# Kernel tuning notes

Hardware: AMD Instinct MI355X
Metric: run time of the kernel (lower is better)

The kernel has to match this reference:

```python
import jax, jax.numpy as jnp
import numpy as np

N_EMBED = 384
T_MAX = 256
EPS = 1e-5


def layer_norm(x, gamma, beta):
    mu = jnp.mean(x, axis=-1, keepdims=True)
    var = jnp.mean(jnp.square(x - mu), axis=-1, keepdims=True)
    return (x - mu) * jax.lax.rsqrt(var + EPS) * gamma + beta


def setup_inputs() -> dict:
    key = jax.random.key(0)
    ks = jax.random.split(key, 12)
    B, T, C = 128, 256, N_EMBED
    s = lambda fan_in: 1.0 / np.sqrt(fan_in)
    return {
        "x": jax.random.normal(ks[0], (B, T, C), dtype=jnp.float32),
        "W_attn": jax.random.uniform(ks[1], (C, 3 * C), minval=-s(C), maxval=s(C), dtype=jnp.float32),
        "b_attn": jax.random.uniform(ks[2], (3 * C,), minval=-s(C), maxval=s(C), dtype=jnp.float32),
        "W_proj": jax.random.uniform(ks[3], (C, C), minval=-s(C), maxval=s(C), dtype=jnp.float32),
        "b_proj": jax.random.uniform(ks[4], (C,), minval=-s(C), maxval=s(C), dtype=jnp.float32),
        "ln1_g": jnp.ones((C,), jnp.float32),
        "ln1_b": jnp.zeros((C,), jnp.float32),
        "ln2_g": jnp.ones((C,), jnp.float32),
        "ln2_b": jnp.zeros((C,), jnp.float32),
        "W1": jax.random.uniform(ks[5], (C, 4 * C), minval=-s(C), maxval=s(C), dtype=jnp.float32),
        "b1": jax.random.uniform(ks[6], (4 * C,), minval=-s(C), maxval=s(C), dtype=jnp.float32),
        "W2": jax.random.uniform(ks[7], (4 * C, C), minval=-s(4 * C), maxval=s(4 * C), dtype=jnp.float32),
        "b2": jax.random.uniform(ks[8], (4 * C,)[:1] and (C,), minval=-s(4 * C), maxval=s(4 * C), dtype=jnp.float32),
    }


def reference(x, W_attn, b_attn, W_proj, b_proj, ln1_g, ln1_b, ln2_g, ln2_b, W1, b1, W2, b2):
    B, T, C = x.shape
    # --- pre-LN single-head causal self-attention ---
    h = layer_norm(x, ln1_g, ln1_b)
    qkv = h @ W_attn + b_attn                      # [B,T,3C]
    q, k, v = jnp.split(qkv, 3, axis=-1)           # each [B,T,C]
    att = jnp.einsum('btc,bsc->bts', q, k) * (1.0 / jnp.sqrt(jnp.float32(C)))
    causal = jnp.tril(jnp.ones((T, T), bool))
    att = jnp.where(causal, att, -jnp.inf)
    att = jax.nn.softmax(att, axis=-1)             # dropout is identity (eval)
    y = jnp.einsum('bts,bsc->btc', att, v)
    x = x + (y @ W_proj + b_proj)
    # --- pre-LN MLP ---
    h2 = layer_norm(x, ln2_g, ln2_b)
    x = x + (jax.nn.relu(h2 @ W1 + b1) @ W2 + b2)
    return x
```

## Files before the change

### kernel.cpp

```cpp
#include <hip/hip_runtime.h>
#include <hip/hip_bf16.h>

#define C_EMB 384
#define T_SEQ 256
#define B_BATCH 128
#define M_ROWS (B_BATCH * T_SEQ)
#define QKV_LD 1152
#define BK 64

typedef __bf16 bf16_8 __attribute__((ext_vector_type(8)));
typedef float f32x4 __attribute__((ext_vector_type(4)));

__device__ __forceinline__ void load16_lds(const __bf16* g, __bf16* l) {
    __builtin_amdgcn_global_load_lds(
        (const __attribute__((address_space(1))) unsigned int*)g,
        (__attribute__((address_space(3))) unsigned int*)l, 16, 0, 0);
}

__global__ __launch_bounds__(256) void cast_all_kernel(const float* __restrict__ Wa,
                                                       const float* __restrict__ Wp,
                                                       const float* __restrict__ W1,
                                                       const float* __restrict__ W2,
                                                       __bf16* __restrict__ Wa_t,
                                                       __bf16* __restrict__ Wp_t,
                                                       __bf16* __restrict__ W1_t,
                                                       __bf16* __restrict__ W2_t) {
    int bid = blockIdx.x;
    const float* W; __bf16* Wt; int K, N, tx_n;
    if (bid < 432)      { W = Wa; Wt = Wa_t; K = 384;  N = 1152; tx_n = 36; }
    else if (bid < 576) { bid -= 432; W = Wp; Wt = Wp_t; K = 384;  N = 384;  tx_n = 12; }
    else if (bid < 1152){ bid -= 576; W = W1; Wt = W1_t; K = 384;  N = 1536; tx_n = 48; }
    else                { bid -= 1152; W = W2; Wt = W2_t; K = 1536; N = 384;  tx_n = 12; }
    int n0 = (bid % tx_n) * 32, k0 = (bid / tx_n) * 32;

    __shared__ float t[32][33];
    int tx = threadIdx.x & 31, ty = threadIdx.x >> 5;
#pragma unroll
    for (int i = 0; i < 4; ++i)
        t[ty + i * 8][tx] = W[(size_t)(k0 + ty + i * 8) * N + n0 + tx];
    __syncthreads();
#pragma unroll
    for (int i = 0; i < 4; ++i) {
        int n = ty + i * 8;
        Wt[(size_t)(n0 + n) * K + k0 + tx] = (__bf16)t[tx][n];
    }
}

__global__ __launch_bounds__(384) void ln_kernel(const float* __restrict__ x,
                                                 const float* __restrict__ g,
                                                 const float* __restrict__ bta,
                                                 __bf16* __restrict__ out) {
    int row = blockIdx.x;
    int c = threadIdx.x;
    float v = x[(size_t)row * C_EMB + c];

    __shared__ float red[6];
    float s = v;
#pragma unroll
    for (int o = 32; o; o >>= 1) s += __shfl_down(s, o);
    if ((c & 63) == 0) red[c >> 6] = s;
    __syncthreads();
    float mu = (red[0] + red[1] + red[2] + red[3] + red[4] + red[5]) * (1.0f / C_EMB);

    float d = v - mu;
    float s2 = d * d;
#pragma unroll
    for (int o = 32; o; o >>= 1) s2 += __shfl_down(s2, o);
    __syncthreads();
    if ((c & 63) == 0) red[c >> 6] = s2;
    __syncthreads();
    float var = (red[0] + red[1] + red[2] + red[3] + red[4] + red[5]) * (1.0f / C_EMB);

    out[(size_t)row * C_EMB + c] = (__bf16)(d * rsqrtf(var + 1e-5f) * g[c] + bta[c]);
}

template <int TM, bool RELU, bool RESID, bool OUT_BF16>
__global__ __launch_bounds__(256) void mfma_gemm(const __bf16* __restrict__ A, int lda,
                                                 const __bf16* __restrict__ Bt, int ldb,
                                                 const float* __restrict__ bias,
                                                 const float* __restrict__ resid,
                                                 void* __restrict__ out_,
                                                 int N, int K) {
    constexpr int MI = TM / 32;
    constexpr int WROWS = TM / 2;
    __shared__ __align__(16) __bf16 As[2 * TM * 32];
    __shared__ __align__(16) __bf16 Bs[2 * 128 * 32];

    int tid = threadIdx.x;
    int wave = tid >> 6, lane = tid & 63;
    int wr = wave >> 1, wc = wave & 1;
    int quad = lane >> 4, l16 = lane & 15;
    int bm = blockIdx.y * TM, bn = blockIdx.x * 128;
    int lrow = lane >> 2, lcol = (lane & 3) * 8;

    f32x4 acc[MI][4] = {};

    for (int k0 = 0; k0 < K; k0 += BK) {
        const __bf16* Ab = A + (size_t)bm * lda + k0;
        const __bf16* Bb = Bt + (size_t)bn * ldb + k0;
#pragma unroll
        for (int p = 0; p < 2; ++p) {
#pragma unroll
            for (int i = 0; i < TM / 64; ++i) {
                int r0 = (i * 4 + wave) * 16;
                load16_lds(Ab + (size_t)(r0 + lrow) * lda + p * 32 + lcol,
                           &As[p * TM * 32 + r0 * 32]);
            }
#pragma unroll
            for (int i = 0; i < 2; ++i) {
                int r0 = (i * 4 + wave) * 16;
                load16_lds(Bb + (size_t)(r0 + lrow) * ldb + p * 32 + lcol,
                           &Bs[p * 128 * 32 + r0 * 32]);
            }
        }
        __syncthreads();

        bf16_8 af[MI][2], bf[4][2];
#pragma unroll
        for (int p = 0; p < 2; ++p) {
#pragma unroll
            for (int i = 0; i < MI; ++i)
                af[i][p] = *reinterpret_cast<const bf16_8*>(
                    &As[p * TM * 32 + (wr * WROWS + i * 16 + l16) * 32 + quad * 8]);
#pragma unroll
            for (int j = 0; j < 4; ++j)
                bf[j][p] = *reinterpret_cast<const bf16_8*>(
                    &Bs[p * 128 * 32 + (wc * 64 + j * 16 + l16) * 32 + quad * 8]);
        }
#pragma unroll
        for (int i = 0; i < MI; ++i)
#pragma unroll
            for (int j = 0; j < 4; ++j) {
                acc[i][j] = __builtin_amdgcn_mfma_f32_16x16x32_bf16(af[i][0], bf[j][0], acc[i][j], 0, 0, 0);
                acc[i][j] = __builtin_amdgcn_mfma_f32_16x16x32_bf16(af[i][1], bf[j][1], acc[i][j], 0, 0, 0);
            }
        __syncthreads();
    }

#pragma unroll
    for (int i = 0; i < MI; ++i) {
#pragma unroll
        for (int r = 0; r < 4; ++r) {
            int m = bm + wr * WROWS + i * 16 + quad * 4 + r;
#pragma unroll
            for (int j = 0; j < 4; ++j) {
                int n = bn + wc * 64 + j * 16 + l16;
                float v = acc[i][j][r] + bias[n];
                if (RELU) v = fmaxf(v, 0.0f);
                if (RESID) v += resid[(size_t)m * N + n];
                if (OUT_BF16)
                    ((__bf16*)out_)[(size_t)m * N + n] = (__bf16)v;
                else
                    ((float*)out_)[(size_t)m * N + n] = v;
            }
        }
    }
}

__global__ __launch_bounds__(256) void vt_kernel(const __bf16* __restrict__ qkv,
                                                 __bf16* __restrict__ Vt) {
    __shared__ __align__(16) __bf16 t[32][72];
    int b = blockIdx.z, c0 = blockIdx.x * 64, s0 = blockIdx.y * 32;
    int tid = threadIdx.x;

    int tx = tid & 7, ty = tid >> 3;
    const __bf16* src = qkv + ((size_t)b * T_SEQ + s0 + ty) * QKV_LD + 768 + c0 + tx * 8;
    *reinterpret_cast<float4*>(&t[ty][tx * 8]) = *reinterpret_cast<const float4*>(src);
    __syncthreads();

    int sx = tid & 3, cy = tid >> 2;
    __align__(16) __bf16 tmp[8];
#pragma unroll
    for (int j = 0; j < 8; ++j) tmp[j] = t[sx * 8 + j][cy];
    *reinterpret_cast<float4*>(&Vt[((size_t)b * C_EMB + c0 + cy) * T_SEQ + s0 + sx * 8]) =
        *reinterpret_cast<float4*>(tmp);
}

__global__ __launch_bounds__(256) void qk_mfma(const __bf16* __restrict__ qkv,
                                               float* __restrict__ S) {
    static const int TMt[3] = {0, 1, 1};
    static const int TNt[3] = {0, 0, 1};
    int b = blockIdx.y;
    int bm = TMt[blockIdx.x] * 128, bn = TNt[blockIdx.x] * 128;
    const __bf16* Ab0 = qkv + (size_t)b * T_SEQ * QKV_LD;
    const __bf16* Bb0 = Ab0 + 384;

    __shared__ __align__(16) __bf16 As[2 * 128 * 32];
    __shared__ __align__(16) __bf16 Bs[2 * 128 * 32];

    int tid = threadIdx.x;
    int wave = tid >> 6, lane = tid & 63;
    int wr = wave >> 1, wc = wave & 1;
    int quad = lane >> 4, l16 = lane & 15;
    int lrow = lane >> 2, lcol = (lane & 3) * 8;

    f32x4 acc[4][4] = {};

    for (int k0 = 0; k0 < C_EMB; k0 += BK) {
        const __bf16* Ab = Ab0 + (size_t)bm * QKV_LD + k0;
        const __bf16* Bb = Bb0 + (size_t)bn * QKV_LD + k0;
#pragma unroll
        for (int p = 0; p < 2; ++p)
#pragma unroll
            for (int i = 0; i < 2; ++i) {
                int r0 = (i * 4 + wave) * 16;
                load16_lds(Ab + (size_t)(r0 + lrow) * QKV_LD + p * 32 + lcol,
                           &As[p * 128 * 32 + r0 * 32]);
                load16_lds(Bb + (size_t)(r0 + lrow) * QKV_LD + p * 32 + lcol,
                           &Bs[p * 128 * 32 + r0 * 32]);
            }
        __syncthreads();

        bf16_8 af[4][2], bf[4][2];
#pragma unroll
        for (int p = 0; p < 2; ++p)
#pragma unroll
            for (int i = 0; i < 4; ++i) {
                af[i][p] = *reinterpret_cast<const bf16_8*>(
                    &As[p * 128 * 32 + (wr * 64 + i * 16 + l16) * 32 + quad * 8]);
                bf[i][p] = *reinterpret_cast<const bf16_8*>(
                    &Bs[p * 128 * 32 + (wc * 64 + i * 16 + l16) * 32 + quad * 8]);
            }
#pragma unroll
        for (int i = 0; i < 4; ++i)
#pragma unroll
            for (int j = 0; j < 4; ++j) {
                acc[i][j] = __builtin_amdgcn_mfma_f32_16x16x32_bf16(af[i][0], bf[j][0], acc[i][j], 0, 0, 0);
                acc[i][j] = __builtin_amdgcn_mfma_f32_16x16x32_bf16(af[i][1], bf[j][1], acc[i][j], 0, 0, 0);
            }
        __syncthreads();
    }

    float* Sb = S + (size_t)b * T_SEQ * T_SEQ;
#pragma unroll
    for (int i = 0; i < 4; ++i) {
#pragma unroll
        for (int r = 0; r < 4; ++r) {
            int m = bm + wr * 64 + i * 16 + quad * 4 + r;
#pragma unroll
            for (int j = 0; j < 4; ++j) {
                int n = bn + wc * 64 + j * 16 + l16;
                Sb[(size_t)m * T_SEQ + n] = acc[i][j][r] * 0.05103103630798288f;
            }
        }
    }
}

__global__ __launch_bounds__(256) void softmax_kernel(const float* __restrict__ S,
                                                      __bf16* __restrict__ P) {
    int row = blockIdx.x;
    int t = row & (T_SEQ - 1);
    int tid = threadIdx.x;
    const float* Sr = S + (size_t)row * T_SEQ;

    __shared__ float red[4];
    float sc = (tid <= t) ? Sr[tid] : -INFINITY;

    float mx = sc;
#pragma unroll
    for (int o = 32; o; o >>= 1) mx = fmaxf(mx, __shfl_down(mx, o));
    if ((tid & 63) == 0) red[tid >> 6] = mx;
    __syncthreads();
    mx = fmaxf(fmaxf(red[0], red[1]), fmaxf(red[2], red[3]));

    float p = (tid <= t) ? __expf(sc - mx) : 0.0f;
    float sm = p;
#pragma unroll
    for (int o = 32; o; o >>= 1) sm += __shfl_down(sm, o);
    __syncthreads();
    if ((tid & 63) == 0) red[tid >> 6] = sm;
    __syncthreads();
    sm = red[0] + red[1] + red[2] + red[3];

    P[(size_t)row * T_SEQ + tid] = (__bf16)(p / sm);
}

__global__ __launch_bounds__(256) void pv_mfma(const __bf16* __restrict__ P,
                                               const __bf16* __restrict__ Vt,
                                               __bf16* __restrict__ y) {
    int b = blockIdx.z;
    int bm = blockIdx.y * 128, bn = blockIdx.x * 128;
    const __bf16* Ab0 = P + (size_t)b * T_SEQ * T_SEQ;
    const __bf16* Bb0 = Vt + (size_t)b * C_EMB * T_SEQ;

    __shared__ __align__(16) __bf16 As[2 * 128 * 32];
    __shared__ __align__(16) __bf16 Bs[2 * 128 * 32];

    int tid = threadIdx.x;
    int wave = tid >> 6, lane = tid & 63;
    int wr = wave >> 1, wc = wave & 1;
    int quad = lane >> 4, l16 = lane & 15;
    int lrow = lane >> 2, lcol = (lane & 3) * 8;

    f32x4 acc[4][4] = {};

    int kmax = bm + 128;
    for (int k0 = 0; k0 < kmax; k0 += BK) {
        const __bf16* Ab = Ab0 + (size_t)bm * T_SEQ + k0;
        const __bf16* Bb = Bb0 + (size_t)bn * T_SEQ + k0;
#pragma unroll
        for (int p = 0; p < 2; ++p)
#pragma unroll
            for (int i = 0; i < 2; ++i) {
                int r0 = (i * 4 + wave) * 16;
                load16_lds(Ab + (size_t)(r0 + lrow) * T_SEQ + p * 32 + lcol,
                           &As[p * 128 * 32 + r0 * 32]);
                load16_lds(Bb + (size_t)(r0 + lrow) * T_SEQ + p * 32 + lcol,
                           &Bs[p * 128 * 32 + r0 * 32]);
            }
        __syncthreads();

        bf16_8 af[4][2], bf[4][2];
#pragma unroll
        for (int p = 0; p < 2; ++p)
#pragma unroll
            for (int i = 0; i < 4; ++i) {
                af[i][p] = *reinterpret_cast<const bf16_8*>(
                    &As[p * 128 * 32 + (wr * 64 + i * 16 + l16) * 32 + quad * 8]);
                bf[i][p] = *reinterpret_cast<const bf16_8*>(
                    &Bs[p * 128 * 32 + (wc * 64 + i * 16 + l16) * 32 + quad * 8]);
            }
#pragma unroll
        for (int i = 0; i < 4; ++i)
#pragma unroll
            for (int j = 0; j < 4; ++j) {
                acc[i][j] = __builtin_amdgcn_mfma_f32_16x16x32_bf16(af[i][0], bf[j][0], acc[i][j], 0, 0, 0);
                acc[i][j] = __builtin_amdgcn_mfma_f32_16x16x32_bf16(af[i][1], bf[j][1], acc[i][j], 0, 0, 0);
            }
        __syncthreads();
    }

#pragma unroll
    for (int i = 0; i < 4; ++i) {
#pragma unroll
        for (int r = 0; r < 4; ++r) {
            int m = bm + wr * 64 + i * 16 + quad * 4 + r;
#pragma unroll
            for (int j = 0; j < 4; ++j) {
                int n = bn + wc * 64 + j * 16 + l16;
                y[((size_t)b * T_SEQ + m) * C_EMB + n] = (__bf16)acc[i][j][r];
            }
        }
    }
}

extern "C" void kernel_launch(void* const* d_in, const int* in_sizes, int n_in,
                              void* d_out, int out_size, void* d_ws, size_t ws_size,
                              hipStream_t stream) {
    const float* x      = (const float*)d_in[0];
    const float* W_attn = (const float*)d_in[1];
    const float* b_attn = (const float*)d_in[2];
    const float* W_proj = (const float*)d_in[3];
    const float* b_proj = (const float*)d_in[4];
    const float* ln1_g  = (const float*)d_in[5];
    const float* ln1_b  = (const float*)d_in[6];
    const float* ln2_g  = (const float*)d_in[7];
    const float* ln2_b  = (const float*)d_in[8];
    const float* W1     = (const float*)d_in[9];
    const float* b1     = (const float*)d_in[10];
    const float* W2     = (const float*)d_in[11];
    const float* b2     = (const float*)d_in[12];
    float* out = (float*)d_out;

    __bf16* Wattn_t = (__bf16*)d_ws;
    __bf16* Wproj_t = Wattn_t + (size_t)1152 * 384;
    __bf16* W1_t    = Wproj_t + (size_t)384 * 384;
    __bf16* W2_t    = W1_t + (size_t)1536 * 384;
    __bf16* h       = W2_t + (size_t)384 * 1536;
    __bf16* yb      = h + (size_t)M_ROWS * 384;
    __bf16* qkv     = yb + (size_t)M_ROWS * 384;
    float*  S       = (float*)(qkv + (size_t)M_ROWS * QKV_LD);
    __bf16* Pb      = (__bf16*)(S + (size_t)B_BATCH * T_SEQ * T_SEQ);
    __bf16* Vt      = Pb + (size_t)B_BATCH * T_SEQ * T_SEQ;
    __bf16* ff      = qkv;

    cast_all_kernel<<<1728, 256, 0, stream>>>(W_attn, W_proj, W1, W2,
                                              Wattn_t, Wproj_t, W1_t, W2_t);

    ln_kernel<<<M_ROWS, 384, 0, stream>>>(x, ln1_g, ln1_b, h);
    mfma_gemm<128, false, false, true><<<dim3(1152 / 128, M_ROWS / 128), 256, 0, stream>>>(
        h, 384, Wattn_t, 384, b_attn, nullptr, qkv, 1152, 384);
    vt_kernel<<<dim3(C_EMB / 64, T_SEQ / 32, B_BATCH), 256, 0, stream>>>(qkv, Vt);
    qk_mfma<<<dim3(3, B_BATCH), 256, 0, stream>>>(qkv, S);
    softmax_kernel<<<M_ROWS, 256, 0, stream>>>(S, Pb);
    pv_mfma<<<dim3(C_EMB / 128, T_SEQ / 128, B_BATCH), 256, 0, stream>>>(Pb, Vt, yb);
    mfma_gemm<64, false, true, false><<<dim3(384 / 128, M_ROWS / 64), 256, 0, stream>>>(
        yb, 384, Wproj_t, 384, b_proj, x, out, 384, 384);
    ln_kernel<<<M_ROWS, 384, 0, stream>>>(out, ln2_g, ln2_b, h);
    mfma_gemm<128, true, false, true><<<dim3(1536 / 128, M_ROWS / 128), 256, 0, stream>>>(
        h, 384, W1_t, 384, b1, nullptr, ff, 1536, 384);
    mfma_gemm<64, false, true, false><<<dim3(384 / 128, M_ROWS / 64), 256, 0, stream>>>(
        ff, 1536, W2_t, 1536, b2, out, out, 384, 1536);
}
```

Baseline: 494.7 us.

## Fuse MLP up-projection, ReLU and down-projection into one kernel

Replaces the two MLP GEMM launches with a single kernel that computes a 64-row tile of h2@W1 in 64-column chunks. Each chunk gets bias and ReLU, is staged in LDS as bf16, and is immediately multiplied by the matching W2 slice, accumulating into registers. This removes writing and re-reading the 32768x1536 bf16 intermediate in global memory and one launch. In exchange, the W1/W2 tiles are re-streamed per row block with no double buffering, only 512 blocks run with many sync points, and register pressure is high (24 A fragments plus 24 accumulators per thread).

```diff
diff --git a/kernel.cpp b/kernel.cpp
--- a/kernel.cpp
+++ b/kernel.cpp
@@ -155,6 +155,128 @@
             }
         }
     }
+}
+
+__global__ __launch_bounds__(256, 2) void mlp_fused(const __bf16* __restrict__ h2,
+                                                    const __bf16* __restrict__ W1t,
+                                                    const __bf16* __restrict__ W2t,
+                                                    const float* __restrict__ b1,
+                                                    const float* __restrict__ b2,
+                                                    float* __restrict__ out) {
+    __shared__ __align__(16) __bf16 Bs[24576];
+    __shared__ __align__(16) __bf16 Ps[4096];
+
+    int tid = threadIdx.x;
+    int wave = tid >> 6, lane = tid & 63;
+    int wr = wave >> 1, wc = wave & 1;
+    int quad = lane >> 4, l16 = lane & 15;
+    int bm = blockIdx.x * 64;
+
+    int srow = lane >> 3;
+    int sunit = (lane & 7) ^ srow;
+
+    bf16_8 af1[2][12];
+    {
+        const __bf16* h0 = h2 + (size_t)(bm + wr * 32 + l16) * C_EMB + quad * 8;
+#pragma unroll
+        for (int i = 0; i < 2; ++i)
+#pragma unroll
+            for (int p = 0; p < 12; ++p)
+                af1[i][p] = *reinterpret_cast<const bf16_8*>(h0 + i * 16 * C_EMB + p * 32);
+    }
+
+    f32x4 acc2[2][12] = {};
+
+    for (int c = 0; c < 24; ++c) {
+        __syncthreads();
+        {
+            const __bf16* src = W1t + (size_t)(c * 64 + srow) * C_EMB + sunit * 8;
+#pragma unroll
+            for (int t = 0; t < 12; ++t) {
+                int g = t * 4 + wave;
+                int kp = g >> 3, rg = g & 7;
+                load16_lds(src + (size_t)(rg * 8) * C_EMB + kp * 64,
+                           &Bs[kp * 4096 + rg * 8 * 64]);
+            }
+        }
+        __syncthreads();
+
+        f32x4 pacc[2][2] = {};
+#pragma unroll
+        for (int p = 0; p < 12; ++p) {
+            int kp = p >> 1;
+            bf16_8 bf[2];
+#pragma unroll
+            for (int j = 0; j < 2; ++j) {
+                int row = wc * 32 + j * 16 + l16;
+                int unit = (((p & 1) * 4 + quad) ^ (row & 7));
+                bf[j] = *reinterpret_cast<const bf16_8*>(&Bs[kp * 4096 + row * 64 + unit * 8]);
+            }
+#pragma unroll
+            for (int i = 0; i < 2; ++i)
+#pragma unroll
+                for (int j = 0; j < 2; ++j)
+                    pacc[i][j] = __builtin_amdgcn_mfma_f32_16x16x32_bf16(af1[i][p], bf[j], pacc[i][j], 0, 0, 0);
+        }
+
+        __syncthreads();
+        {
+            const __bf16* src = W2t + (size_t)srow * 1536 + c * 64 + sunit * 8;
+#pragma unroll
+            for (int t = 0; t < 12; ++t) {
+                int g = t * 4 + wave;
+                load16_lds(src + (size_t)(g * 8) * 1536, &Bs[g * 8 * 64]);
+            }
+        }
+#pragma unroll
+        for (int i = 0; i < 2; ++i)
+#pragma unroll
+            for (int j = 0; j < 2; ++j) {
+                int col = wc * 32 + j * 16 + l16;
+                float bb = b1[c * 64 + col];
+                int unit0 = col >> 3, cw = col & 7;
+#pragma unroll
+                for (int r = 0; r < 4; ++r) {
+                    int row = wr * 32 + i * 16 + quad * 4 + r;
+                    float v = fmaxf(pacc[i][j][r] + bb, 0.0f);
+                    Ps[row * 64 + ((unit0 ^ (row & 7)) << 3) + cw] = (__bf16)v;
+                }
+            }
+        __syncthreads();
+
+#pragma unroll
+        for (int p = 0; p < 2; ++p) {
+            bf16_8 pf[2];
+#pragma unroll
+            for (int i = 0; i < 2; ++i) {
+                int row = wr * 32 + i * 16 + l16;
+                int unit = ((p * 4 + quad) ^ (row & 7));
+                pf[i] = *reinterpret_cast<const bf16_8*>(&Ps[row * 64 + unit * 8]);
+            }
+#pragma unroll
+            for (int j = 0; j < 12; ++j) {
+                int row = wc * 192 + j * 16 + l16;
+                int unit = ((p * 4 + quad) ^ (row & 7));
+                bf16_8 bf = *reinterpret_cast<const bf16_8*>(&Bs[row * 64 + unit * 8]);
+#pragma unroll
+                for (int i = 0; i < 2; ++i)
+                    acc2[i][j] = __builtin_amdgcn_mfma_f32_16x16x32_bf16(pf[i], bf, acc2[i][j], 0, 0, 0);
+            }
+        }
+    }
+
+#pragma unroll
+    for (int i = 0; i < 2; ++i)
+#pragma unroll
+        for (int r = 0; r < 4; ++r) {
+            int m = bm + wr * 32 + i * 16 + quad * 4 + r;
+#pragma unroll
+            for (int j = 0; j < 12; ++j) {
+                int n = wc * 192 + j * 16 + l16;
+                float* o = &out[(size_t)m * C_EMB + n];
+                *o = *o + acc2[i][j][r] + b2[n];
+            }
+        }
 }
 
 __global__ __launch_bounds__(256) void vt_kernel(const __bf16* __restrict__ qkv,
@@ -372,7 +494,6 @@
     float*  S       = (float*)(qkv + (size_t)M_ROWS * QKV_LD);
     __bf16* Pb      = (__bf16*)(S + (size_t)B_BATCH * T_SEQ * T_SEQ);
     __bf16* Vt      = Pb + (size_t)B_BATCH * T_SEQ * T_SEQ;
-    __bf16* ff      = qkv;
 
     cast_all_kernel<<<1728, 256, 0, stream>>>(W_attn, W_proj, W1, W2,
                                               Wattn_t, Wproj_t, W1_t, W2_t);
@@ -387,8 +508,5 @@
     mfma_gemm<64, false, true, false><<<dim3(384 / 128, M_ROWS / 64), 256, 0, stream>>>(
         yb, 384, Wproj_t, 384, b_proj, x, out, 384, 384);
     ln_kernel<<<M_ROWS, 384, 0, stream>>>(out, ln2_g, ln2_b, h);
-    mfma_gemm<128, true, false, true><<<dim3(1536 / 128, M_ROWS / 128), 256, 0, stream>>>(
-        h, 384, W1_t, 384, b1, nullptr, ff, 1536, 384);
-    mfma_gemm<64, false, true, false><<<dim3(384 / 128, M_ROWS / 64), 256, 0, stream>>>(
-        ff, 1536, W2_t, 1536, b2, out, out, 384, 1536);
-}
+    mlp_fused<<<M_ROWS / 64, 256, 0, stream>>>(h, W1_t, W2_t, b1, b2, out);
+}
```

New measurement: 537.3 us. 8.6% more time.

## Fuse causal QK^T scoring with softmax into a single MFMA kernel

Applied to the files above, without the earlier changes.

Merges the QK^T GEMM and the row-softmax into one kernel. Each block now owns a 128-row strip and computes every causal key tile for it, keeping the scores in registers. Row max and row sum are reduced with shuffles plus a small LDS exchange, and the normalized bf16 probabilities are written directly. This removes the fp32 score matrix round-trip through global memory and one kernel launch. In exchange the grid shrinks to two unequal-work blocks per batch, the accumulator register footprint doubles, and the fully masked upper tile of P for the first strip is no longer written with zeros.

```diff
diff --git a/kernel.cpp b/kernel.cpp
--- a/kernel.cpp
+++ b/kernel.cpp
@@ -176,17 +176,18 @@
         *reinterpret_cast<float4*>(tmp);
 }
 
-__global__ __launch_bounds__(256) void qk_mfma(const __bf16* __restrict__ qkv,
-                                               float* __restrict__ S) {
-    static const int TMt[3] = {0, 1, 1};
-    static const int TNt[3] = {0, 0, 1};
+__global__ __launch_bounds__(256) void qks_mfma(const __bf16* __restrict__ qkv,
+                                                __bf16* __restrict__ P) {
     int b = blockIdx.y;
-    int bm = TMt[blockIdx.x] * 128, bn = TNt[blockIdx.x] * 128;
+    int bx = blockIdx.x;
+    int bm = bx * 128;
+    int ntiles = bx + 1;
     const __bf16* Ab0 = qkv + (size_t)b * T_SEQ * QKV_LD;
     const __bf16* Bb0 = Ab0 + 384;
 
     __shared__ __align__(16) __bf16 As[2 * 128 * 32];
     __shared__ __align__(16) __bf16 Bs[2 * 128 * 32];
+    __shared__ float red[2][2][128];
 
     int tid = threadIdx.x;
     int wave = tid >> 6, lane = tid & 63;
@@ -194,85 +195,123 @@
     int quad = lane >> 4, l16 = lane & 15;
     int lrow = lane >> 2, lcol = (lane & 3) * 8;
 
-    f32x4 acc[4][4] = {};
-
-    for (int k0 = 0; k0 < C_EMB; k0 += BK) {
-        const __bf16* Ab = Ab0 + (size_t)bm * QKV_LD + k0;
-        const __bf16* Bb = Bb0 + (size_t)bn * QKV_LD + k0;
-#pragma unroll
-        for (int p = 0; p < 2; ++p)
-#pragma unroll
-            for (int i = 0; i < 2; ++i) {
-                int r0 = (i * 4 + wave) * 16;
-                load16_lds(Ab + (size_t)(r0 + lrow) * QKV_LD + p * 32 + lcol,
-                           &As[p * 128 * 32 + r0 * 32]);
-                load16_lds(Bb + (size_t)(r0 + lrow) * QKV_LD + p * 32 + lcol,
-                           &Bs[p * 128 * 32 + r0 * 32]);
-            }
-        __syncthreads();
-
-        bf16_8 af[4][2], bf[4][2];
-#pragma unroll
-        for (int p = 0; p < 2; ++p)
-#pragma unroll
-            for (int i = 0; i < 4; ++i) {
-                af[i][p] = *reinterpret_cast<const bf16_8*>(
-                    &As[p * 128 * 32 + (wr * 64 + i * 16 + l16) * 32 + quad * 8]);
-                bf[i][p] = *reinterpret_cast<const bf16_8*>(
-                    &Bs[p * 128 * 32 + (wc * 64 + i * 16 + l16) * 32 + quad * 8]);
-            }
+    f32x4 acc[2][4][4] = {};
+
+    for (int nt = 0; nt < ntiles; ++nt) {
+        int bn = nt * 128;
+        for (int k0 = 0; k0 < C_EMB; k0 += BK) {
+            const __bf16* Ab = Ab0 + (size_t)bm * QKV_LD + k0;
+            const __bf16* Bb = Bb0 + (size_t)bn * QKV_LD + k0;
+#pragma unroll
+            for (int p = 0; p < 2; ++p)
+#pragma unroll
+                for (int i = 0; i < 2; ++i) {
+                    int r0 = (i * 4 + wave) * 16;
+                    load16_lds(Ab + (size_t)(r0 + lrow) * QKV_LD + p * 32 + lcol,
+                               &As[p * 128 * 32 + r0 * 32]);
+                    load16_lds(Bb + (size_t)(r0 + lrow) * QKV_LD + p * 32 + lcol,
+                               &Bs[p * 128 * 32 + r0 * 32]);
+                }
+            __syncthreads();
+
+            bf16_8 af[4][2], bf[4][2];
+#pragma unroll
+            for (int p = 0; p < 2; ++p)
+#pragma unroll
+                for (int i = 0; i < 4; ++i) {
+                    af[i][p] = *reinterpret_cast<const bf16_8*>(
+                        &As[p * 128 * 32 + (wr * 64 + i * 16 + l16) * 32 + quad * 8]);
+                    bf[i][p] = *reinterpret_cast<const bf16_8*>(
+                        &Bs[p * 128 * 32 + (wc * 64 + i * 16 + l16) * 32 + quad * 8]);
+                }
+#pragma unroll
+            for (int i = 0; i < 4; ++i)
+#pragma unroll
+                for (int j = 0; j < 4; ++j) {
+                    acc[nt][i][j] = __builtin_amdgcn_mfma_f32_16x16x32_bf16(af[i][0], bf[j][0], acc[nt][i][j], 0, 0, 0);
+                    acc[nt][i][j] = __builtin_amdgcn_mfma_f32_16x16x32_bf16(af[i][1], bf[j][1], acc[nt][i][j], 0, 0, 0);
+                }
+            __syncthreads();
+        }
+    }
+
+    const float scale = 0.05103103630798288f;
+
+    float pm[4][4];
+#pragma unroll
+    for (int i = 0; i < 4; ++i)
+#pragma unroll
+        for (int r = 0; r < 4; ++r) {
+            int t = bm + wr * 64 + i * 16 + quad * 4 + r;
+            float m = -INFINITY;
+#pragma unroll
+            for (int nt = 0; nt < 2; ++nt)
+#pragma unroll
+                for (int j = 0; j < 4; ++j) {
+                    int n = nt * 128 + wc * 64 + j * 16 + l16;
+                    bool ok = (nt < ntiles) && (n <= t);
+                    float v = acc[nt][i][j][r] * scale;
+                    m = fmaxf(m, ok ? v : -INFINITY);
+                }
+#pragma unroll
+            for (int o = 8; o; o >>= 1) m = fmaxf(m, __shfl_xor(m, o));
+            pm[i][r] = m;
+        }
+    if (l16 == 0) {
 #pragma unroll
         for (int i = 0; i < 4; ++i)
 #pragma unroll
-            for (int j = 0; j < 4; ++j) {
-                acc[i][j] = __builtin_amdgcn_mfma_f32_16x16x32_bf16(af[i][0], bf[j][0], acc[i][j], 0, 0, 0);
-                acc[i][j] = __builtin_amdgcn_mfma_f32_16x16x32_bf16(af[i][1], bf[j][1], acc[i][j], 0, 0, 0);
-            }
-        __syncthreads();
-    }
-
-    float* Sb = S + (size_t)b * T_SEQ * T_SEQ;
-#pragma unroll
-    for (int i = 0; i < 4; ++i) {
+            for (int r = 0; r < 4; ++r)
+                red[0][wc][wr * 64 + i * 16 + quad * 4 + r] = pm[i][r];
+    }
+    __syncthreads();
+
+    float ps[4][4];
+#pragma unroll
+    for (int i = 0; i < 4; ++i)
 #pragma unroll
         for (int r = 0; r < 4; ++r) {
-            int m = bm + wr * 64 + i * 16 + quad * 4 + r;
-#pragma unroll
-            for (int j = 0; j < 4; ++j) {
-                int n = bn + wc * 64 + j * 16 + l16;
-                Sb[(size_t)m * T_SEQ + n] = acc[i][j][r] * 0.05103103630798288f;
-            }
-        }
-    }
-}
-
-__global__ __launch_bounds__(256) void softmax_kernel(const float* __restrict__ S,
-                                                      __bf16* __restrict__ P) {
-    int row = blockIdx.x;
-    int t = row & (T_SEQ - 1);
-    int tid = threadIdx.x;
-    const float* Sr = S + (size_t)row * T_SEQ;
-
-    __shared__ float red[4];
-    float sc = (tid <= t) ? Sr[tid] : -INFINITY;
-
-    float mx = sc;
-#pragma unroll
-    for (int o = 32; o; o >>= 1) mx = fmaxf(mx, __shfl_down(mx, o));
-    if ((tid & 63) == 0) red[tid >> 6] = mx;
-    __syncthreads();
-    mx = fmaxf(fmaxf(red[0], red[1]), fmaxf(red[2], red[3]));
-
-    float p = (tid <= t) ? __expf(sc - mx) : 0.0f;
-    float sm = p;
-#pragma unroll
-    for (int o = 32; o; o >>= 1) sm += __shfl_down(sm, o);
-    __syncthreads();
-    if ((tid & 63) == 0) red[tid >> 6] = sm;
-    __syncthreads();
-    sm = red[0] + red[1] + red[2] + red[3];
-
-    P[(size_t)row * T_SEQ + tid] = (__bf16)(p / sm);
+            int rloc = wr * 64 + i * 16 + quad * 4 + r;
+            int t = bm + rloc;
+            float M = fmaxf(red[0][0][rloc], red[0][1][rloc]);
+            float s = 0.0f;
+#pragma unroll
+            for (int nt = 0; nt < 2; ++nt)
+#pragma unroll
+                for (int j = 0; j < 4; ++j) {
+                    int n = nt * 128 + wc * 64 + j * 16 + l16;
+                    bool ok = (nt < ntiles) && (n <= t);
+                    float p = ok ? __expf(acc[nt][i][j][r] * scale - M) : 0.0f;
+                    acc[nt][i][j][r] = p;
+                    s += p;
+                }
+#pragma unroll
+            for (int o = 8; o; o >>= 1) s += __shfl_xor(s, o);
+            ps[i][r] = s;
+        }
+    if (l16 == 0) {
+#pragma unroll
+        for (int i = 0; i < 4; ++i)
+#pragma unroll
+            for (int r = 0; r < 4; ++r)
+                red[1][wc][wr * 64 + i * 16 + quad * 4 + r] = ps[i][r];
+    }
+    __syncthreads();
+
+    __bf16* Pb_ = P + (size_t)b * T_SEQ * T_SEQ;
+#pragma unroll
+    for (int i = 0; i < 4; ++i)
+#pragma unroll
+        for (int r = 0; r < 4; ++r) {
+            int rloc = wr * 64 + i * 16 + quad * 4 + r;
+            float inv = 1.0f / (red[1][0][rloc] + red[1][1][rloc]);
+            for (int nt = 0; nt < ntiles; ++nt)
+#pragma unroll
+                for (int j = 0; j < 4; ++j) {
+                    int n = nt * 128 + wc * 64 + j * 16 + l16;
+                    Pb_[(size_t)(bm + rloc) * T_SEQ + n] = (__bf16)(acc[nt][i][j][r] * inv);
+                }
+        }
 }
 
 __global__ __launch_bounds__(256) void pv_mfma(const __bf16* __restrict__ P,
@@ -381,8 +420,7 @@
     mfma_gemm<128, false, false, true><<<dim3(1152 / 128, M_ROWS / 128), 256, 0, stream>>>(
         h, 384, Wattn_t, 384, b_attn, nullptr, qkv, 1152, 384);
     vt_kernel<<<dim3(C_EMB / 64, T_SEQ / 32, B_BATCH), 256, 0, stream>>>(qkv, Vt);
-    qk_mfma<<<dim3(3, B_BATCH), 256, 0, stream>>>(qkv, S);
-    softmax_kernel<<<M_ROWS, 256, 0, stream>>>(S, Pb);
+    qks_mfma<<<dim3(2, B_BATCH), 256, 0, stream>>>(qkv, Pb);
     pv_mfma<<<dim3(C_EMB / 128, T_SEQ / 128, B_BATCH), 256, 0, stream>>>(Pb, Vt, yb);
     mfma_gemm<64, false, true, false><<<dim3(384 / 128, M_ROWS / 64), 256, 0, stream>>>(
         yb, 384, Wproj_t, 384, b_proj, x, out, 384, 384);
```

Result: slower. 578.2 us (+16.9%).
